# Performance work log

Measured on AMD Instinct MI355X. Metric: run time of the kernel, lower is better.

Reference implementation:

```python
import jax, jax.numpy as jnp
import numpy as np


def _lstm(x, Wih, Whh, bih, bhh):
    # x: (T, B, F); Wih: (4H, F); Whh: (4H, H); torch gate order i, f, g, o
    T, B, _ = x.shape
    H = Whh.shape[1]
    # precompute input projections for all timesteps (one big GEMM)
    xg = jnp.einsum('tbf,gf->tbg', x, Wih) + bih + bhh  # (T, B, 4H)

    def step(carry, gx):
        h, c = carry
        g = gx + h @ Whh.T  # (B, 4H)
        i, f, gg, o = jnp.split(g, 4, axis=-1)
        i = jax.nn.sigmoid(i)
        f = jax.nn.sigmoid(f)
        gg = jnp.tanh(gg)
        o = jax.nn.sigmoid(o)
        c = f * c + i * gg
        h = o * jnp.tanh(c)
        return (h, c), h

    h0 = jnp.zeros((B, H), x.dtype)
    (_, _), out = jax.lax.scan(step, (h0, h0), xg)
    return out  # (T, B, H)


def setup_inputs() -> dict:
    key = jax.random.key(0)
    ks = jax.random.split(key, 20)
    T, B, F = 1024, 512, 32
    H1, H2, H3 = 32, 8, 8  # lstm1 hidden=32, lstm2 hidden=8, lstm3 hidden=out_features=8
    p = 0.25
    s = 0.1  # weight init scale

    def mk_mask(k, h):
        keep = (jax.random.uniform(k, (B, h)) > p).astype(jnp.float32)
        return keep / (1.0 - p)

    return {
        'x': jax.random.normal(ks[0], (T, B, F), jnp.float32),
        'W_ih1': jax.random.normal(ks[1], (4 * H1, F)) * s,
        'W_hh1': jax.random.normal(ks[2], (4 * H1, H1)) * s,
        'b_ih1': jax.random.normal(ks[3], (4 * H1,)) * s,
        'b_hh1': jax.random.normal(ks[4], (4 * H1,)) * s,
        'W_ih2': jax.random.normal(ks[5], (4 * H2, H1)) * s,
        'W_hh2': jax.random.normal(ks[6], (4 * H2, H2)) * s,
        'b_ih2': jax.random.normal(ks[7], (4 * H2,)) * s,
        'b_hh2': jax.random.normal(ks[8], (4 * H2,)) * s,
        'W_ih3': jax.random.normal(ks[9], (4 * H3, H2)) * s,
        'W_hh3': jax.random.normal(ks[10], (4 * H3, H3)) * s,
        'b_ih3': jax.random.normal(ks[11], (4 * H3,)) * s,
        'b_hh3': jax.random.normal(ks[12], (4 * H3,)) * s,
        'mask1': mk_mask(ks[13], H1),
        'mask2': mk_mask(ks[14], H2),
        'mask3': mk_mask(ks[15], H3),
    }


def reference(x, W_ih1, W_hh1, b_ih1, b_hh1,
              W_ih2, W_hh2, b_ih2, b_hh2,
              W_ih3, W_hh3, b_ih3, b_hh3,
              mask1, mask2, mask3):
    # Locked (variational) output dropout: one mask per sequence, broadcast over time.
    out = _lstm(x, W_ih1, W_hh1, b_ih1, b_hh1) * mask1[None, :, :]
    out = _lstm(out, W_ih2, W_hh2, b_ih2, b_hh2) * mask2[None, :, :]
    out = _lstm(out, W_ih3, W_hh3, b_ih3, b_hh3) * mask3[None, :, :]
    return out  # (T, B, out_features)
```

## Files before the change

kernel.cpp:

```cpp
#include <hip/hip_runtime.h>


constexpr int T = 1024, B = 512, F = 32;
constexpr int H1 = 32, H2 = 8, H3 = 8;
constexpr int G1 = 4 * H1;
constexpr int HR = 128;
constexpr int XR = 64;
constexpr int OUT_STRIDE = B * H3;

typedef float f32x2 __attribute__((ext_vector_type(2)));
typedef unsigned int u32x2 __attribute__((ext_vector_type(2)));

#define PIN(v) asm volatile("" : "+v"(v))

#if __has_builtin(__builtin_amdgcn_rcpf)
#define RCPF(x) __builtin_amdgcn_rcpf(x)
#else
#define RCPF(x) (1.0f / (x))
#endif
#if __has_builtin(__builtin_amdgcn_exp2f)
#define EXP2F(x) __builtin_amdgcn_exp2f(x)
#else
#define EXP2F(x) exp2f(x)
#endif

#if __has_builtin(__builtin_amdgcn_permlane32_swap)
#define HAVE_PLSWAP 1
#else
#define HAVE_PLSWAP 0
#endif

#define SIG_CM (-1.4426950408889634f)

__device__ __forceinline__ float act_f(float v, float cm, float ka, float kb) {
    return fmaf(ka, RCPF(1.0f + EXP2F(v * cm)), kb);
}
__device__ __forceinline__ float tanh_fast(float v) {
    return fmaf(2.0f, RCPF(1.0f + EXP2F(v * (2.0f * SIG_CM))), -1.0f);
}

__device__ __forceinline__ void pkfma(f32x2& acc, f32x2 a, f32x2 b) {
    acc += a * b;
}

#define LDS_ACQ(p)    __hip_atomic_load((p), __ATOMIC_ACQUIRE, __HIP_MEMORY_SCOPE_WORKGROUP)
#define LDS_REL(p, v) __hip_atomic_store((p), (v), __ATOMIC_RELEASE, __HIP_MEMORY_SCOPE_WORKGROUP)
#define SPIN_UNTIL(EXPR)                                                       \
    do {                                                                       \
        int _g = 0;                                                            \
        while (!(EXPR)) {                                                      \
            __builtin_amdgcn_s_sleep(2);                                       \
            if (++_g > (1 << 22)) break;                                       \
        }                                                                      \
    } while (0)

__global__ __launch_bounds__(192, 1) void lstm3_fused_kernel(
    const float* __restrict__ x,
    const float* __restrict__ Wih1, const float* __restrict__ Whh1,
    const float* __restrict__ bih1, const float* __restrict__ bhh1,
    const float* __restrict__ Wih2, const float* __restrict__ Whh2,
    const float* __restrict__ bih2, const float* __restrict__ bhh2,
    const float* __restrict__ Wih3, const float* __restrict__ Whh3,
    const float* __restrict__ bih3, const float* __restrict__ bhh3,
    const float* __restrict__ mask1, const float* __restrict__ mask2,
    const float* __restrict__ mask3,
    float* __restrict__ out)
{
    const int tid = threadIdx.x;
    const int lane = tid & 63;
    const int wid = tid >> 6;
    const int b = blockIdx.x;

    __shared__ __align__(16) float h1ring[HR][H1];
    __shared__ __align__(16) float xgring[XR][G1];
    __shared__ __align__(16) float xstage[32][F];
    __shared__ __align__(16) float sh23[2][16];
    __shared__ int prog0, prog1, prog2;

    if (tid == 0) { prog0 = 0; prog1 = 0; prog2 = 0; }
    if (wid == 0 && lane < H1) h1ring[HR - 1][lane] = 0.f;
    if (wid == 1 && lane < 16) { sh23[0][lane] = 0.f; sh23[1][lane] = 0.f; }
    __syncthreads();

    if (wid == 2) {
        f32x2 wi0[16], wi1[16];
#pragma unroll
        for (int k = 0; k < 16; ++k) {
            wi0[k] = f32x2{Wih1[lane * F + 2 * k], Wih1[lane * F + 2 * k + 1]};
            wi1[k] = f32x2{Wih1[(lane + 64) * F + 2 * k], Wih1[(lane + 64) * F + 2 * k + 1]};
        }
        const float bias0 = bih1[lane] + bhh1[lane];
        const float bias1 = bih1[lane + 64] + bhh1[lane + 64];
#pragma unroll
        for (int k = 0; k < 16; ++k) { PIN(wi0[k]); PIN(wi1[k]); }

        const float4* x4 = (const float4*)x;
        float4* xr4 = (float4*)xstage;
        const int ttq = lane >> 3, ffq = lane & 7;

        float4 sA = x4[(size_t)(0 + ttq) * 4096 + b * 8 + ffq];
        float4 sB = x4[(size_t)(8 + ttq) * 4096 + b * 8 + ffq];
        xr4[(ttq & 31) * 8 + ffq] = sA;
        xr4[((8 + ttq) & 31) * 8 + ffq] = sB;
        sA = x4[(size_t)(16 + ttq) * 4096 + b * 8 + ffq];
        sB = x4[(size_t)(24 + ttq) * 4096 + b * 8 + ffq];

        for (int t = 0; t < T; ++t) {
            if ((t & 15) == 0) {
                const int need = t - 40;
                if (need > 0) SPIN_UNTIL(LDS_ACQ(&prog0) >= need);
                const int wt = t + 16;
                if (wt < T) {
                    xr4[((wt + ttq) & 31) * 8 + ffq] = sA;
                    xr4[((wt + 8 + ttq) & 31) * 8 + ffq] = sB;
                    const int lt = t + 32;
                    if (lt < T) {
                        sA = x4[(size_t)(lt + ttq) * 4096 + b * 8 + ffq];
                        sB = x4[(size_t)(lt + 8 + ttq) * 4096 + b * 8 + ffq];
                    }
                }
            }
            const float4* xp = (const float4*)xstage[t & 31];
            f32x2 aA = f32x2{bias0, 0.f}, aB = f32x2{0.f, 0.f};
            f32x2 cA = f32x2{bias1, 0.f}, cB = f32x2{0.f, 0.f};
#pragma unroll
            for (int q = 0; q < 8; ++q) {
                const float4 v = xp[q];
                const f32x2 lo = f32x2{v.x, v.y}, hi = f32x2{v.z, v.w};
                pkfma(aA, wi0[2 * q], lo); pkfma(aB, wi0[2 * q + 1], hi);
                pkfma(cA, wi1[2 * q], lo); pkfma(cB, wi1[2 * q + 1], hi);
            }
            const f32x2 sa = aA + aB, sc = cA + cB;
            xgring[t & (XR - 1)][lane] = sa.x + sa.y;
            xgring[t & (XR - 1)][lane + 64] = sc.x + sc.y;
            if ((t & 15) == 15) LDS_REL(&prog2, t + 1);
        }
    } else if (wid == 0) {
        f32x2 w0[16], w1[16];
#pragma unroll
        for (int k = 0; k < 16; ++k) {
            w0[k] = f32x2{Whh1[lane * H1 + 2 * k], Whh1[lane * H1 + 2 * k + 1]};
            w1[k] = f32x2{Whh1[(lane + 64) * H1 + 2 * k], Whh1[(lane + 64) * H1 + 2 * k + 1]};
        }
#pragma unroll
        for (int k = 0; k < 16; ++k) { PIN(w0[k]); PIN(w1[k]); }
        const float cm1 = (lane < 32) ? 2.0f * SIG_CM : SIG_CM;
        const float ka1 = (lane < 32) ? 2.0f : 1.0f;
        const float kb1 = (lane < 32) ? -1.0f : 0.0f;
        float c1 = 0.f;

        SPIN_UNTIL(LDS_ACQ(&prog2) >= ((34 < T) ? 34 : T));
        float pa = xgring[0][lane], pb = xgring[0][lane + 64];
        float na = xgring[1][lane], nb = xgring[1][lane + 64];

        for (int i = 0; i < T; ++i) {
            if ((i & 31) == 0 && i) {
                int tgt = i + 34; if (tgt > T) tgt = T;
                SPIN_UNTIL(LDS_ACQ(&prog2) >= tgt);
            }
            if ((i & 63) == 0 && i >= 64)
                SPIN_UNTIL(LDS_ACQ(&prog1) >= i - 48);

            const float4* h1p = (const float4*)h1ring[(i - 1) & (HR - 1)];
            f32x2 A0 = f32x2{0.f, 0.f}, A1 = f32x2{0.f, 0.f};
            f32x2 B0 = f32x2{0.f, 0.f}, B1 = f32x2{0.f, 0.f};
#pragma unroll
            for (int q = 0; q < 8; ++q) {
                const float4 v = h1p[q];
                const f32x2 lo = f32x2{v.x, v.y}, hi = f32x2{v.z, v.w};
                pkfma(A0, w0[2 * q], lo); pkfma(A1, w0[2 * q + 1], hi);
                pkfma(B0, w1[2 * q], lo); pkfma(B1, w1[2 * q + 1], hi);
            }
            const f32x2 SA = A0 + A1, SB = B0 + B1;
            const float a0 = pa + (SA.x + SA.y);
            const float a1 = pb + (SB.x + SB.y);
            const float g0 = act_f(a0, SIG_CM, 1.0f, 0.0f);
            const float g1 = act_f(a1, cm1, ka1, kb1);
            pa = na; pb = nb;
            {
                int tn = i + 2; if (tn > T - 1) tn = T - 1;
                na = xgring[tn & (XR - 1)][lane];
                nb = xgring[tn & (XR - 1)][lane + 64];
            }
            float h1v;
#if HAVE_PLSWAP
            const u32x2 pif = __builtin_amdgcn_permlane32_swap(
                __float_as_uint(g0), __float_as_uint(g0), false, false);
            const u32x2 pgo = __builtin_amdgcn_permlane32_swap(
                __float_as_uint(g1), __float_as_uint(g1), false, false);
            const float iv = __uint_as_float(pif.x);
            const float fv = __uint_as_float(pif.y);
            const float gv = __uint_as_float(pgo.x);
            const float ov = __uint_as_float(pgo.y);
            c1 = fmaf(fv, c1, iv * gv);
            h1v = ov * tanh_fast(c1);
#else
            const float fv = __shfl_xor(g0, 32);
            const float ov = __shfl_xor(g1, 32);
            c1 = fmaf(fv, c1, g0 * g1);
            h1v = ov * tanh_fast(c1);
#endif
            if (lane < H1) h1ring[i & (HR - 1)][lane] = h1v;
            if ((i & 7) == 7) LDS_REL(&prog0, i + 1);
        }
    } else {
        f32x2 wp[24];
        float biasX, m3;
        const int r = lane & 31;
        const bool lower = (lane < 32);
        if (lower) {
#pragma unroll
            for (int k = 0; k < 16; ++k)
                wp[k] = f32x2{Wih2[r * H1 + 2 * k] * mask1[b * H1 + 2 * k],
                              Wih2[r * H1 + 2 * k + 1] * mask1[b * H1 + 2 * k + 1]};
#pragma unroll
            for (int k = 0; k < 4; ++k)
                wp[16 + k] = f32x2{Whh2[r * H2 + 2 * k], Whh2[r * H2 + 2 * k + 1]};
#pragma unroll
            for (int k = 0; k < 4; ++k) wp[20 + k] = f32x2{0.f, 0.f};
            biasX = bih2[r] + bhh2[r];
        } else {
#pragma unroll
            for (int k = 0; k < 16; ++k) wp[k] = f32x2{0.f, 0.f};
#pragma unroll
            for (int k = 0; k < 4; ++k)
                wp[16 + k] = f32x2{Wih3[r * H2 + 2 * k] * mask2[b * H2 + 2 * k],
                                   Wih3[r * H2 + 2 * k + 1] * mask2[b * H2 + 2 * k + 1]};
#pragma unroll
            for (int k = 0; k < 4; ++k)
                wp[20 + k] = f32x2{Whh3[r * H3 + 2 * k], Whh3[r * H3 + 2 * k + 1]};
            biasX = bih3[r] + bhh3[r];
        }
        const int sec = r >> 3;
        const float cmX = (sec == 2) ? 2.0f * SIG_CM : SIG_CM;
        const float kaX = (sec == 2) ? 2.0f : 1.0f;
        const float kbX = (sec == 2) ? -1.0f : 0.0f;
        m3 = mask3[b * H3 + (lane & 7)];
        const int thresh = lower ? 1 : 2;
        const int gbase = (lane & 32) + (lane & 7);
        const int bx0 = 4 * (gbase + 0),  bx1 = 4 * (gbase + 8);
        const int bx2 = 4 * (gbase + 16), bx3 = 4 * (gbase + 24);
#pragma unroll
        for (int k = 0; k < 24; ++k) PIN(wp[k]);

        float c23 = 0.f;
        for (int i = 0; i <= T + 1; ++i) {
            if ((i & 7) == 0) {
                int tgt = i + 7; if (tgt > T) tgt = T;
                SPIN_UNTIL(LDS_ACQ(&prog0) >= tgt);
            }
            const int par = i & 1;
            const float4* h1p = (const float4*)h1ring[(i - 1) & (HR - 1)];
            const float4* up = (const float4*)sh23[par ^ 1];
            f32x2 s0 = f32x2{0.f, 0.f}, s1 = f32x2{0.f, 0.f};
            f32x2 s2 = f32x2{0.f, 0.f}, s3 = f32x2{0.f, 0.f};
#pragma unroll
            for (int q = 0; q < 4; ++q) {
                const float4 v = h1p[q], w = h1p[q + 4];
                pkfma(s0, wp[2 * q], f32x2{v.x, v.y});
                pkfma(s0, wp[2 * q + 1], f32x2{v.z, v.w});
                pkfma(s1, wp[8 + 2 * q], f32x2{w.x, w.y});
                pkfma(s1, wp[8 + 2 * q + 1], f32x2{w.z, w.w});
            }
            {
                const float4 u0 = up[0], u1 = up[1], u2 = up[2], u3 = up[3];
                pkfma(s2, wp[16], f32x2{u0.x, u0.y});
                pkfma(s2, wp[17], f32x2{u0.z, u0.w});
                pkfma(s2, wp[18], f32x2{u1.x, u1.y});
                pkfma(s2, wp[19], f32x2{u1.z, u1.w});
                pkfma(s3, wp[20], f32x2{u2.x, u2.y});
                pkfma(s3, wp[21], f32x2{u2.z, u2.w});
                pkfma(s3, wp[22], f32x2{u3.x, u3.y});
                pkfma(s3, wp[23], f32x2{u3.z, u3.w});
            }
            const f32x2 st = (s0 + s1) + (s2 + s3);
            const float a23 = biasX + st.x + st.y;
            const float rv = act_f(a23, cmX, kaX, kbX);
            float gi, gf, gg, go;
            asm volatile(
                "ds_bpermute_b32 %0, %4, %8\n\t"
                "ds_bpermute_b32 %1, %5, %8\n\t"
                "ds_bpermute_b32 %2, %6, %8\n\t"
                "ds_bpermute_b32 %3, %7, %8\n\t"
                "s_waitcnt lgkmcnt(0)"
                : "=&v"(gi), "=&v"(gf), "=&v"(gg), "=&v"(go)
                : "v"(bx0), "v"(bx1), "v"(bx2), "v"(bx3), "v"(rv));
            c23 = (i >= thresh) ? fmaf(gf, c23, gi * gg) : 0.0f;
            const float hnew = go * tanh_fast(c23);
            if (i >= 2 && (lane & 56) == 32)
                out[(size_t)(i - 2) * OUT_STRIDE + b * H3 + (lane & 7)] = hnew * m3;
            if ((lane & 24) == 0)
                sh23[par][(lane & 7) | ((lane & 32) >> 2)] = hnew;
            if ((i & 15) == 15) LDS_REL(&prog1, i + 1);
        }
    }
}

extern "C" void kernel_launch(void* const* d_in, const int* in_sizes, int n_in,
                              void* d_out, int out_size, void* d_ws, size_t ws_size,
                              hipStream_t stream) {
    (void)in_sizes; (void)n_in; (void)out_size; (void)d_ws; (void)ws_size;
    const float* x     = (const float*)d_in[0];
    const float* Wih1  = (const float*)d_in[1];
    const float* Whh1  = (const float*)d_in[2];
    const float* bih1  = (const float*)d_in[3];
    const float* bhh1  = (const float*)d_in[4];
    const float* Wih2  = (const float*)d_in[5];
    const float* Whh2  = (const float*)d_in[6];
    const float* bih2  = (const float*)d_in[7];
    const float* bhh2  = (const float*)d_in[8];
    const float* Wih3  = (const float*)d_in[9];
    const float* Whh3  = (const float*)d_in[10];
    const float* bih3  = (const float*)d_in[11];
    const float* bhh3  = (const float*)d_in[12];
    const float* mask1 = (const float*)d_in[13];
    const float* mask2 = (const float*)d_in[14];
    const float* mask3 = (const float*)d_in[15];
    float* out = (float*)d_out;

    lstm3_fused_kernel<<<dim3(B), dim3(192), 0, stream>>>(
        x, Wih1, Whh1, bih1, bhh1,
        Wih2, Whh2, bih2, bhh2,
        Wih3, Whh3, bih3, bhh3,
        mask1, mask2, mask3, out);
}
```

Measured before the change: 539.2 us.

## Broadcast recurrent hidden state via readlane instead of LDS round-trips

The layer-1 recurrence now takes h from the previous step's own registers, broadcasting each element with readlane (SGPR) instead of storing h1 to LDS and reading it back. The layer-2/3 wavefront does the same for its recurrent state, which removes the sh23 LDS exchange. That wavefront also prefetches the next h1 row one iteration early and waits for one extra step of layer-1 progress. The aim is to take LDS write-then-read latency off the serial dependency chain, at the cost of many scalar readlane instructions per step and scalar FMAs in place of packed ones.

```diff
diff --git a/kernel.cpp b/kernel.cpp
--- a/kernel.cpp
+++ b/kernel.cpp
@@ -28,6 +28,12 @@
 #define HAVE_PLSWAP 1
 #else
 #define HAVE_PLSWAP 0
+#endif
+
+#if __has_builtin(__builtin_amdgcn_readlane)
+#define RLF(v, l) __uint_as_float(__builtin_amdgcn_readlane(__float_as_uint(v), (l)))
+#else
+#define RLF(v, l) __shfl((v), (l))
 #endif
 
 #define SIG_CM (-1.4426950408889634f)
@@ -74,12 +80,10 @@
     __shared__ __align__(16) float h1ring[HR][H1];
     __shared__ __align__(16) float xgring[XR][G1];
     __shared__ __align__(16) float xstage[32][F];
-    __shared__ __align__(16) float sh23[2][16];
     __shared__ int prog0, prog1, prog2;
 
     if (tid == 0) { prog0 = 0; prog1 = 0; prog2 = 0; }
     if (wid == 0 && lane < H1) h1ring[HR - 1][lane] = 0.f;
-    if (wid == 1 && lane < 16) { sh23[0][lane] = 0.f; sh23[1][lane] = 0.f; }
     __syncthreads();
 
     if (wid == 2) {
@@ -136,18 +140,18 @@
             if ((t & 15) == 15) LDS_REL(&prog2, t + 1);
         }
     } else if (wid == 0) {
-        f32x2 w0[16], w1[16];
-#pragma unroll
-        for (int k = 0; k < 16; ++k) {
-            w0[k] = f32x2{Whh1[lane * H1 + 2 * k], Whh1[lane * H1 + 2 * k + 1]};
-            w1[k] = f32x2{Whh1[(lane + 64) * H1 + 2 * k], Whh1[(lane + 64) * H1 + 2 * k + 1]};
-        }
-#pragma unroll
-        for (int k = 0; k < 16; ++k) { PIN(w0[k]); PIN(w1[k]); }
+        float w0[H1], w1[H1];
+#pragma unroll
+        for (int k = 0; k < H1; ++k) w0[k] = Whh1[lane * H1 + k];
+#pragma unroll
+        for (int k = 0; k < H1; ++k) w1[k] = Whh1[(lane + 64) * H1 + k];
+#pragma unroll
+        for (int k = 0; k < H1; ++k) { PIN(w0[k]); PIN(w1[k]); }
         const float cm1 = (lane < 32) ? 2.0f * SIG_CM : SIG_CM;
         const float ka1 = (lane < 32) ? 2.0f : 1.0f;
         const float kb1 = (lane < 32) ? -1.0f : 0.0f;
         float c1 = 0.f;
+        float h1v = 0.f;
 
         SPIN_UNTIL(LDS_ACQ(&prog2) >= ((34 < T) ? 34 : T));
         float pa = xgring[0][lane], pb = xgring[0][lane + 64];
@@ -161,19 +165,25 @@
             if ((i & 63) == 0 && i >= 64)
                 SPIN_UNTIL(LDS_ACQ(&prog1) >= i - 48);
 
-            const float4* h1p = (const float4*)h1ring[(i - 1) & (HR - 1)];
-            f32x2 A0 = f32x2{0.f, 0.f}, A1 = f32x2{0.f, 0.f};
-            f32x2 B0 = f32x2{0.f, 0.f}, B1 = f32x2{0.f, 0.f};
-#pragma unroll
-            for (int q = 0; q < 8; ++q) {
-                const float4 v = h1p[q];
-                const f32x2 lo = f32x2{v.x, v.y}, hi = f32x2{v.z, v.w};
-                pkfma(A0, w0[2 * q], lo); pkfma(A1, w0[2 * q + 1], hi);
-                pkfma(B0, w1[2 * q], lo); pkfma(B1, w1[2 * q + 1], hi);
-            }
-            const f32x2 SA = A0 + A1, SB = B0 + B1;
-            const float a0 = pa + (SA.x + SA.y);
-            const float a1 = pb + (SB.x + SB.y);
+            float a0A = 0.f, a0B = 0.f, a0C = 0.f, a0D = 0.f;
+            float a1A = 0.f, a1B = 0.f, a1C = 0.f, a1D = 0.f;
+#pragma unroll
+            for (int k = 0; k < 8; ++k) {
+                const float s0 = RLF(h1v, k);
+                const float s1 = RLF(h1v, k + 8);
+                const float s2 = RLF(h1v, k + 16);
+                const float s3 = RLF(h1v, k + 24);
+                a0A = fmaf(s0, w0[k],      a0A);
+                a0B = fmaf(s1, w0[k + 8],  a0B);
+                a0C = fmaf(s2, w0[k + 16], a0C);
+                a0D = fmaf(s3, w0[k + 24], a0D);
+                a1A = fmaf(s0, w1[k],      a1A);
+                a1B = fmaf(s1, w1[k + 8],  a1B);
+                a1C = fmaf(s2, w1[k + 16], a1C);
+                a1D = fmaf(s3, w1[k + 24], a1D);
+            }
+            const float a0 = pa + ((a0A + a0B) + (a0C + a0D));
+            const float a1 = pb + ((a1A + a1B) + (a1C + a1D));
             const float g0 = act_f(a0, SIG_CM, 1.0f, 0.0f);
             const float g1 = act_f(a1, cm1, ka1, kb1);
             pa = na; pb = nb;
@@ -182,7 +192,6 @@
                 na = xgring[tn & (XR - 1)][lane];
                 nb = xgring[tn & (XR - 1)][lane + 64];
             }
-            float h1v;
 #if HAVE_PLSWAP
             const u32x2 pif = __builtin_amdgcn_permlane32_swap(
                 __float_as_uint(g0), __float_as_uint(g0), false, false);
@@ -204,7 +213,8 @@
             if ((i & 7) == 7) LDS_REL(&prog0, i + 1);
         }
     } else {
-        f32x2 wp[24];
+        f32x2 wp[16];
+        float wu[16];
         float biasX, m3;
         const int r = lane & 31;
         const bool lower = (lane < 32);
@@ -214,21 +224,17 @@
                 wp[k] = f32x2{Wih2[r * H1 + 2 * k] * mask1[b * H1 + 2 * k],
                               Wih2[r * H1 + 2 * k + 1] * mask1[b * H1 + 2 * k + 1]};
 #pragma unroll
-            for (int k = 0; k < 4; ++k)
-                wp[16 + k] = f32x2{Whh2[r * H2 + 2 * k], Whh2[r * H2 + 2 * k + 1]};
-#pragma unroll
-            for (int k = 0; k < 4; ++k) wp[20 + k] = f32x2{0.f, 0.f};
+            for (int k = 0; k < H2; ++k) wu[k] = Whh2[r * H2 + k];
+#pragma unroll
+            for (int k = 0; k < H3; ++k) wu[8 + k] = 0.0f;
             biasX = bih2[r] + bhh2[r];
         } else {
 #pragma unroll
             for (int k = 0; k < 16; ++k) wp[k] = f32x2{0.f, 0.f};
 #pragma unroll
-            for (int k = 0; k < 4; ++k)
-                wp[16 + k] = f32x2{Wih3[r * H2 + 2 * k] * mask2[b * H2 + 2 * k],
-                                   Wih3[r * H2 + 2 * k + 1] * mask2[b * H2 + 2 * k + 1]};
-#pragma unroll
-            for (int k = 0; k < 4; ++k)
-                wp[20 + k] = f32x2{Whh3[r * H3 + 2 * k], Whh3[r * H3 + 2 * k + 1]};
+            for (int k = 0; k < H2; ++k) wu[k] = Wih3[r * H2 + k] * mask2[b * H2 + k];
+#pragma unroll
+            for (int k = 0; k < H3; ++k) wu[8 + k] = Whh3[r * H3 + k];
             biasX = bih3[r] + bhh3[r];
         }
         const int sec = r >> 3;
@@ -241,40 +247,41 @@
         const int bx0 = 4 * (gbase + 0),  bx1 = 4 * (gbase + 8);
         const int bx2 = 4 * (gbase + 16), bx3 = 4 * (gbase + 24);
 #pragma unroll
-        for (int k = 0; k < 24; ++k) PIN(wp[k]);
+        for (int k = 0; k < 16; ++k) { PIN(wp[k]); PIN(wu[k]); }
 
         float c23 = 0.f;
+        float hprev = 0.f;
+        const float4* hp0 = (const float4*)h1ring[HR - 1];
+        float4 hq0 = hp0[0], hq1 = hp0[1], hq2 = hp0[2], hq3 = hp0[3];
+        float4 hq4 = hp0[4], hq5 = hp0[5], hq6 = hp0[6], hq7 = hp0[7];
+
         for (int i = 0; i <= T + 1; ++i) {
             if ((i & 7) == 0) {
-                int tgt = i + 7; if (tgt > T) tgt = T;
+                int tgt = i + 8; if (tgt > T) tgt = T;
                 SPIN_UNTIL(LDS_ACQ(&prog0) >= tgt);
             }
-            const int par = i & 1;
-            const float4* h1p = (const float4*)h1ring[(i - 1) & (HR - 1)];
-            const float4* up = (const float4*)sh23[par ^ 1];
+            float uA = 0.f, uB = 0.f;
+#pragma unroll
+            for (int k = 0; k < 8; ++k) {
+                uA = fmaf(RLF(hprev, k),      wu[k],     uA);
+                uB = fmaf(RLF(hprev, 32 + k), wu[8 + k], uB);
+            }
             f32x2 s0 = f32x2{0.f, 0.f}, s1 = f32x2{0.f, 0.f};
-            f32x2 s2 = f32x2{0.f, 0.f}, s3 = f32x2{0.f, 0.f};
-#pragma unroll
-            for (int q = 0; q < 4; ++q) {
-                const float4 v = h1p[q], w = h1p[q + 4];
-                pkfma(s0, wp[2 * q], f32x2{v.x, v.y});
-                pkfma(s0, wp[2 * q + 1], f32x2{v.z, v.w});
-                pkfma(s1, wp[8 + 2 * q], f32x2{w.x, w.y});
-                pkfma(s1, wp[8 + 2 * q + 1], f32x2{w.z, w.w});
-            }
+            pkfma(s0, wp[0], f32x2{hq0.x, hq0.y}); pkfma(s0, wp[1], f32x2{hq0.z, hq0.w});
+            pkfma(s0, wp[2], f32x2{hq1.x, hq1.y}); pkfma(s0, wp[3], f32x2{hq1.z, hq1.w});
+            pkfma(s0, wp[4], f32x2{hq2.x, hq2.y}); pkfma(s0, wp[5], f32x2{hq2.z, hq2.w});
+            pkfma(s0, wp[6], f32x2{hq3.x, hq3.y}); pkfma(s0, wp[7], f32x2{hq3.z, hq3.w});
+            pkfma(s1, wp[8], f32x2{hq4.x, hq4.y}); pkfma(s1, wp[9], f32x2{hq4.z, hq4.w});
+            pkfma(s1, wp[10], f32x2{hq5.x, hq5.y}); pkfma(s1, wp[11], f32x2{hq5.z, hq5.w});
+            pkfma(s1, wp[12], f32x2{hq6.x, hq6.y}); pkfma(s1, wp[13], f32x2{hq6.z, hq6.w});
+            pkfma(s1, wp[14], f32x2{hq7.x, hq7.y}); pkfma(s1, wp[15], f32x2{hq7.z, hq7.w});
             {
-                const float4 u0 = up[0], u1 = up[1], u2 = up[2], u3 = up[3];
-                pkfma(s2, wp[16], f32x2{u0.x, u0.y});
-                pkfma(s2, wp[17], f32x2{u0.z, u0.w});
-                pkfma(s2, wp[18], f32x2{u1.x, u1.y});
-                pkfma(s2, wp[19], f32x2{u1.z, u1.w});
-                pkfma(s3, wp[20], f32x2{u2.x, u2.y});
-                pkfma(s3, wp[21], f32x2{u2.z, u2.w});
-                pkfma(s3, wp[22], f32x2{u3.x, u3.y});
-                pkfma(s3, wp[23], f32x2{u3.z, u3.w});
-            }
-            const f32x2 st = (s0 + s1) + (s2 + s3);
-            const float a23 = biasX + st.x + st.y;
+                const float4* hp = (const float4*)h1ring[i & (HR - 1)];
+                hq0 = hp[0]; hq1 = hp[1]; hq2 = hp[2]; hq3 = hp[3];
+                hq4 = hp[4]; hq5 = hp[5]; hq6 = hp[6]; hq7 = hp[7];
+            }
+            const f32x2 sh = s0 + s1;
+            const float a23 = biasX + (sh.x + sh.y) + (uA + uB);
             const float rv = act_f(a23, cmX, kaX, kbX);
             float gi, gf, gg, go;
             asm volatile(
@@ -289,8 +296,7 @@
             const float hnew = go * tanh_fast(c23);
             if (i >= 2 && (lane & 56) == 32)
                 out[(size_t)(i - 2) * OUT_STRIDE + b * H3 + (lane & 7)] = hnew * m3;
-            if ((lane & 24) == 0)
-                sh23[par][(lane & 7) | ((lane & 32) >> 2)] = hnew;
+            hprev = hnew;
             if ((i & 15) == 15) LDS_REL(&prog1, i + 1);
         }
     }
```

New measurement: 622.2 us. 15.4% more time.

## Fold activation scale constants into weights and prefetch h1 rows for layers 2/3

Applied to the files above, without the earlier changes.

Pre-multiplies the input/recurrent weights and biases by the sigmoid/tanh exp2 scale constants, so the serial recurrence no longer needs a multiply before each exp2. The cell state is kept in scaled form, which lets the tanh be written as a single fma. The layer-2/3 wave loads the next h1 row into registers after the current step's math, taking LDS latency off the critical path, and its wait target moves up by one. Accumulators are split into more independent chains to shorten dependency depth, at the cost of extra registers and slightly different float rounding.

```diff
diff --git a/kernel.cpp b/kernel.cpp
--- a/kernel.cpp
+++ b/kernel.cpp
@@ -31,13 +31,6 @@
 #endif
 
 #define SIG_CM (-1.4426950408889634f)
-
-__device__ __forceinline__ float act_f(float v, float cm, float ka, float kb) {
-    return fmaf(ka, RCPF(1.0f + EXP2F(v * cm)), kb);
-}
-__device__ __forceinline__ float tanh_fast(float v) {
-    return fmaf(2.0f, RCPF(1.0f + EXP2F(v * (2.0f * SIG_CM))), -1.0f);
-}
 
 __device__ __forceinline__ void pkfma(f32x2& acc, f32x2 a, f32x2 b) {
     acc += a * b;
@@ -83,14 +76,16 @@
     __syncthreads();
 
     if (wid == 2) {
+        const float cmA = SIG_CM;
+        const float cmB = (lane < 32) ? 2.0f * SIG_CM : SIG_CM;
         f32x2 wi0[16], wi1[16];
 #pragma unroll
         for (int k = 0; k < 16; ++k) {
-            wi0[k] = f32x2{Wih1[lane * F + 2 * k], Wih1[lane * F + 2 * k + 1]};
-            wi1[k] = f32x2{Wih1[(lane + 64) * F + 2 * k], Wih1[(lane + 64) * F + 2 * k + 1]};
-        }
-        const float bias0 = bih1[lane] + bhh1[lane];
-        const float bias1 = bih1[lane + 64] + bhh1[lane + 64];
+            wi0[k] = f32x2{Wih1[lane * F + 2 * k] * cmA, Wih1[lane * F + 2 * k + 1] * cmA};
+            wi1[k] = f32x2{Wih1[(lane + 64) * F + 2 * k] * cmB, Wih1[(lane + 64) * F + 2 * k + 1] * cmB};
+        }
+        const float bias0 = (bih1[lane] + bhh1[lane]) * cmA;
+        const float bias1 = (bih1[lane + 64] + bhh1[lane + 64]) * cmB;
 #pragma unroll
         for (int k = 0; k < 16; ++k) { PIN(wi0[k]); PIN(wi1[k]); }
 
@@ -136,18 +131,19 @@
             if ((t & 15) == 15) LDS_REL(&prog2, t + 1);
         }
     } else if (wid == 0) {
+        const float s1d = 2.0f * SIG_CM;
+        const float cm1 = (lane < 32) ? 2.0f * SIG_CM : SIG_CM;
         f32x2 w0[16], w1[16];
 #pragma unroll
         for (int k = 0; k < 16; ++k) {
-            w0[k] = f32x2{Whh1[lane * H1 + 2 * k], Whh1[lane * H1 + 2 * k + 1]};
-            w1[k] = f32x2{Whh1[(lane + 64) * H1 + 2 * k], Whh1[(lane + 64) * H1 + 2 * k + 1]};
+            w0[k] = f32x2{Whh1[lane * H1 + 2 * k] * SIG_CM, Whh1[lane * H1 + 2 * k + 1] * SIG_CM};
+            w1[k] = f32x2{Whh1[(lane + 64) * H1 + 2 * k] * cm1, Whh1[(lane + 64) * H1 + 2 * k + 1] * cm1};
         }
 #pragma unroll
         for (int k = 0; k < 16; ++k) { PIN(w0[k]); PIN(w1[k]); }
-        const float cm1 = (lane < 32) ? 2.0f * SIG_CM : SIG_CM;
-        const float ka1 = (lane < 32) ? 2.0f : 1.0f;
-        const float kb1 = (lane < 32) ? -1.0f : 0.0f;
-        float c1 = 0.f;
+        const float ka1 = (lane < 32) ? (s1d + s1d) : 1.0f;
+        const float kb1 = (lane < 32) ? -s1d : 0.0f;
+        float c1s = 0.f;
 
         SPIN_UNTIL(LDS_ACQ(&prog2) >= ((34 < T) ? 34 : T));
         float pa = xgring[0][lane], pb = xgring[0][lane + 64];
@@ -162,20 +158,34 @@
                 SPIN_UNTIL(LDS_ACQ(&prog1) >= i - 48);
 
             const float4* h1p = (const float4*)h1ring[(i - 1) & (HR - 1)];
-            f32x2 A0 = f32x2{0.f, 0.f}, A1 = f32x2{0.f, 0.f};
-            f32x2 B0 = f32x2{0.f, 0.f}, B1 = f32x2{0.f, 0.f};
+            f32x2 hp2[16];
 #pragma unroll
             for (int q = 0; q < 8; ++q) {
                 const float4 v = h1p[q];
-                const f32x2 lo = f32x2{v.x, v.y}, hi = f32x2{v.z, v.w};
-                pkfma(A0, w0[2 * q], lo); pkfma(A1, w0[2 * q + 1], hi);
-                pkfma(B0, w1[2 * q], lo); pkfma(B1, w1[2 * q + 1], hi);
-            }
-            const f32x2 SA = A0 + A1, SB = B0 + B1;
-            const float a0 = pa + (SA.x + SA.y);
-            const float a1 = pb + (SB.x + SB.y);
-            const float g0 = act_f(a0, SIG_CM, 1.0f, 0.0f);
-            const float g1 = act_f(a1, cm1, ka1, kb1);
+                hp2[2 * q] = f32x2{v.x, v.y};
+                hp2[2 * q + 1] = f32x2{v.z, v.w};
+            }
+            f32x2 A0 = f32x2{pa, 0.f}, A1 = f32x2{0.f, 0.f};
+            f32x2 A2 = f32x2{0.f, 0.f}, A3 = f32x2{0.f, 0.f};
+            f32x2 B0 = f32x2{pb, 0.f}, B1 = f32x2{0.f, 0.f};
+            f32x2 B2 = f32x2{0.f, 0.f}, B3 = f32x2{0.f, 0.f};
+#pragma unroll
+            for (int d = 0; d < 4; ++d) {
+                pkfma(A0, w0[0 + 4 * d], hp2[0 + 4 * d]);
+                pkfma(A1, w0[1 + 4 * d], hp2[1 + 4 * d]);
+                pkfma(A2, w0[2 + 4 * d], hp2[2 + 4 * d]);
+                pkfma(A3, w0[3 + 4 * d], hp2[3 + 4 * d]);
+                pkfma(B0, w1[0 + 4 * d], hp2[0 + 4 * d]);
+                pkfma(B1, w1[1 + 4 * d], hp2[1 + 4 * d]);
+                pkfma(B2, w1[2 + 4 * d], hp2[2 + 4 * d]);
+                pkfma(B3, w1[3 + 4 * d], hp2[3 + 4 * d]);
+            }
+            const f32x2 SA = (A0 + A1) + (A2 + A3);
+            const f32x2 SB = (B0 + B1) + (B2 + B3);
+            const float a0s = SA.x + SA.y;
+            const float a1s = SB.x + SB.y;
+            const float g0 = RCPF(1.0f + EXP2F(a0s));
+            const float g1 = fmaf(ka1, RCPF(1.0f + EXP2F(a1s)), kb1);
             pa = na; pb = nb;
             {
                 int tn = i + 2; if (tn > T - 1) tn = T - 1;
@@ -190,92 +200,112 @@
                 __float_as_uint(g1), __float_as_uint(g1), false, false);
             const float iv = __uint_as_float(pif.x);
             const float fv = __uint_as_float(pif.y);
-            const float gv = __uint_as_float(pgo.x);
+            const float gsv = __uint_as_float(pgo.x);
             const float ov = __uint_as_float(pgo.y);
-            c1 = fmaf(fv, c1, iv * gv);
-            h1v = ov * tanh_fast(c1);
+            c1s = fmaf(fv, c1s, iv * gsv);
+            const float rt = RCPF(1.0f + EXP2F(c1s));
+            h1v = fmaf(ov + ov, rt, -ov);
 #else
             const float fv = __shfl_xor(g0, 32);
             const float ov = __shfl_xor(g1, 32);
-            c1 = fmaf(fv, c1, g0 * g1);
-            h1v = ov * tanh_fast(c1);
+            c1s = fmaf(fv, c1s, g0 * g1);
+            const float rt = RCPF(1.0f + EXP2F(c1s));
+            h1v = fmaf(ov + ov, rt, -ov);
 #endif
             if (lane < H1) h1ring[i & (HR - 1)][lane] = h1v;
             if ((i & 7) == 7) LDS_REL(&prog0, i + 1);
         }
     } else {
-        f32x2 wp[24];
-        float biasX, m3;
+        const float sX = 2.0f * SIG_CM;
         const int r = lane & 31;
         const bool lower = (lane < 32);
+        const int sec = r >> 3;
+        const float cmX = (sec == 2) ? sX : SIG_CM;
+        const float kaX = (sec == 2) ? (sX + sX) : 1.0f;
+        const float kbX = (sec == 2) ? -sX : 0.0f;
+        f32x2 wp[16];
+        f32x2 wup[8];
+        float biasX, m3;
         if (lower) {
 #pragma unroll
             for (int k = 0; k < 16; ++k)
-                wp[k] = f32x2{Wih2[r * H1 + 2 * k] * mask1[b * H1 + 2 * k],
-                              Wih2[r * H1 + 2 * k + 1] * mask1[b * H1 + 2 * k + 1]};
+                wp[k] = f32x2{Wih2[r * H1 + 2 * k] * mask1[b * H1 + 2 * k] * cmX,
+                              Wih2[r * H1 + 2 * k + 1] * mask1[b * H1 + 2 * k + 1] * cmX};
 #pragma unroll
             for (int k = 0; k < 4; ++k)
-                wp[16 + k] = f32x2{Whh2[r * H2 + 2 * k], Whh2[r * H2 + 2 * k + 1]};
-#pragma unroll
-            for (int k = 0; k < 4; ++k) wp[20 + k] = f32x2{0.f, 0.f};
-            biasX = bih2[r] + bhh2[r];
+                wup[k] = f32x2{Whh2[r * H2 + 2 * k] * cmX, Whh2[r * H2 + 2 * k + 1] * cmX};
+#pragma unroll
+            for (int k = 0; k < 4; ++k) wup[4 + k] = f32x2{0.f, 0.f};
+            biasX = (bih2[r] + bhh2[r]) * cmX;
         } else {
 #pragma unroll
             for (int k = 0; k < 16; ++k) wp[k] = f32x2{0.f, 0.f};
 #pragma unroll
             for (int k = 0; k < 4; ++k)
-                wp[16 + k] = f32x2{Wih3[r * H2 + 2 * k] * mask2[b * H2 + 2 * k],
-                                   Wih3[r * H2 + 2 * k + 1] * mask2[b * H2 + 2 * k + 1]};
+                wup[k] = f32x2{Wih3[r * H2 + 2 * k] * mask2[b * H2 + 2 * k] * cmX,
+                               Wih3[r * H2 + 2 * k + 1] * mask2[b * H2 + 2 * k + 1] * cmX};
 #pragma unroll
             for (int k = 0; k < 4; ++k)
-                wp[20 + k] = f32x2{Whh3[r * H3 + 2 * k], Whh3[r * H3 + 2 * k + 1]};
-            biasX = bih3[r] + bhh3[r];
-        }
-        const int sec = r >> 3;
-        const float cmX = (sec == 2) ? 2.0f * SIG_CM : SIG_CM;
-        const float kaX = (sec == 2) ? 2.0f : 1.0f;
-        const float kbX = (sec == 2) ? -1.0f : 0.0f;
+                wup[4 + k] = f32x2{Whh3[r * H3 + 2 * k] * cmX, Whh3[r * H3 + 2 * k + 1] * cmX};
+            biasX = (bih3[r] + bhh3[r]) * cmX;
+        }
         m3 = mask3[b * H3 + (lane & 7)];
         const int thresh = lower ? 1 : 2;
         const int gbase = (lane & 32) + (lane & 7);
         const int bx0 = 4 * (gbase + 0),  bx1 = 4 * (gbase + 8);
         const int bx2 = 4 * (gbase + 16), bx3 = 4 * (gbase + 24);
 #pragma unroll
-        for (int k = 0; k < 24; ++k) PIN(wp[k]);
-
-        float c23 = 0.f;
+        for (int k = 0; k < 16; ++k) PIN(wp[k]);
+#pragma unroll
+        for (int k = 0; k < 8; ++k) PIN(wup[k]);
+
+        float c23s = 0.f;
+        f32x2 hq2[16];
+        {
+            const float4* hp0 = (const float4*)h1ring[HR - 1];
+#pragma unroll
+            for (int q = 0; q < 8; ++q) {
+                const float4 v = hp0[q];
+                hq2[2 * q] = f32x2{v.x, v.y};
+                hq2[2 * q + 1] = f32x2{v.z, v.w};
+            }
+        }
+
         for (int i = 0; i <= T + 1; ++i) {
             if ((i & 7) == 0) {
-                int tgt = i + 7; if (tgt > T) tgt = T;
+                int tgt = i + 8; if (tgt > T) tgt = T;
                 SPIN_UNTIL(LDS_ACQ(&prog0) >= tgt);
             }
             const int par = i & 1;
-            const float4* h1p = (const float4*)h1ring[(i - 1) & (HR - 1)];
             const float4* up = (const float4*)sh23[par ^ 1];
-            f32x2 s0 = f32x2{0.f, 0.f}, s1 = f32x2{0.f, 0.f};
-            f32x2 s2 = f32x2{0.f, 0.f}, s3 = f32x2{0.f, 0.f};
-#pragma unroll
-            for (int q = 0; q < 4; ++q) {
-                const float4 v = h1p[q], w = h1p[q + 4];
-                pkfma(s0, wp[2 * q], f32x2{v.x, v.y});
-                pkfma(s0, wp[2 * q + 1], f32x2{v.z, v.w});
-                pkfma(s1, wp[8 + 2 * q], f32x2{w.x, w.y});
-                pkfma(s1, wp[8 + 2 * q + 1], f32x2{w.z, w.w});
+            const float4 u0 = up[0], u1 = up[1], u2 = up[2], u3 = up[3];
+            f32x2 S0 = f32x2{biasX, 0.f}, S1 = f32x2{0.f, 0.f};
+            f32x2 S2 = f32x2{0.f, 0.f}, S3 = f32x2{0.f, 0.f};
+#pragma unroll
+            for (int d = 0; d < 4; ++d) {
+                pkfma(S0, wp[0 + 4 * d], hq2[0 + 4 * d]);
+                pkfma(S1, wp[1 + 4 * d], hq2[1 + 4 * d]);
+                pkfma(S2, wp[2 + 4 * d], hq2[2 + 4 * d]);
+                pkfma(S3, wp[3 + 4 * d], hq2[3 + 4 * d]);
             }
             {
-                const float4 u0 = up[0], u1 = up[1], u2 = up[2], u3 = up[3];
-                pkfma(s2, wp[16], f32x2{u0.x, u0.y});
-                pkfma(s2, wp[17], f32x2{u0.z, u0.w});
-                pkfma(s2, wp[18], f32x2{u1.x, u1.y});
-                pkfma(s2, wp[19], f32x2{u1.z, u1.w});
-                pkfma(s3, wp[20], f32x2{u2.x, u2.y});
-                pkfma(s3, wp[21], f32x2{u2.z, u2.w});
-                pkfma(s3, wp[22], f32x2{u3.x, u3.y});
-                pkfma(s3, wp[23], f32x2{u3.z, u3.w});
-            }
-            const f32x2 st = (s0 + s1) + (s2 + s3);
-            const float a23 = biasX + st.x + st.y;
-            const float rv = act_f(a23, cmX, kaX, kbX);
+                const float4* hp = (const float4*)h1ring[i & (HR - 1)];
+#pragma unroll
+                for (int q = 0; q < 8; ++q) {
+                    const float4 v = hp[q];
+                    hq2[2 * q] = f32x2{v.x, v.y};
+                    hq2[2 * q + 1] = f32x2{v.z, v.w};
+                }
+            }
+            f32x2 U0 = f32x2{0.f, 0.f}, U1 = f32x2{0.f, 0.f};
+            f32x2 U2 = f32x2{0.f, 0.f}, U3 = f32x2{0.f, 0.f};
+            pkfma(U0, wup[0], f32x2{u0.x, u0.y}); pkfma(U0, wup[4], f32x2{u2.x, u2.y});
+            pkfma(U1, wup[1], f32x2{u0.z, u0.w}); pkfma(U1, wup[5], f32x2{u2.z, u2.w});
+            pkfma(U2, wup[2], f32x2{u1.x, u1.y}); pkfma(U2, wup[6], f32x2{u3.x, u3.y});
+            pkfma(U3, wup[3], f32x2{u1.z, u1.w}); pkfma(U3, wup[7], f32x2{u3.z, u3.w});
+            const f32x2 ST = ((S0 + S1) + (S2 + S3)) + ((U0 + U1) + (U2 + U3));
+            const float a23s = ST.x + ST.y;
+            const float rv = fmaf(kaX, RCPF(1.0f + EXP2F(a23s)), kbX);
             float gi, gf, gg, go;
             asm volatile(
                 "ds_bpermute_b32 %0, %4, %8\n\t"
@@ -285,8 +315,9 @@
                 "s_waitcnt lgkmcnt(0)"
                 : "=&v"(gi), "=&v"(gf), "=&v"(gg), "=&v"(go)
                 : "v"(bx0), "v"(bx1), "v"(bx2), "v"(bx3), "v"(rv));
-            c23 = (i >= thresh) ? fmaf(gf, c23, gi * gg) : 0.0f;
-            const float hnew = go * tanh_fast(c23);
+            c23s = (i >= thresh) ? fmaf(gf, c23s, gi * gg) : 0.0f;
+            const float rt = RCPF(1.0f + EXP2F(c23s));
+            const float hnew = fmaf(go + go, rt, -go);
             if (i >= 2 && (lane & 56) == 32)
                 out[(size_t)(i - 2) * OUT_STRIDE + b * H3 + (lane & 7)] = hnew * m3;
             if ((lane & 24) == 0)
```

After: 513.0 us. 4.9% less time.
